# Kernel tuning notes

Measured on AMD Instinct MI355X. Metric: run time of the kernel, lower is better.

## Reference

```python
import jax, jax.numpy as jnp
import numpy as np

NUM_CLASSES = 1000
GAMMA = 0.9
N = 131072


def setup_inputs() -> dict:
    key = jax.random.key(0)
    k1, k2, k3 = jax.random.split(key, 3)
    preds = jax.random.normal(k1, (N, NUM_CLASSES), dtype=jnp.float32)
    labels = jax.random.randint(k2, (N,), 0, NUM_CLASSES)
    val_preds = jax.random.normal(k3, (NUM_CLASSES, NUM_CLASSES), dtype=jnp.float32)
    return {"preds": preds, "labels": labels, "val_preds": val_preds}


def reference(preds, labels, val_preds):
    # Equivalent of ValScores.update: per-class mean of preds (label-indexed
    # segment reduction) followed by an EMA update, skipping empty classes.
    C = val_preds.shape[0]
    # sums[c] = sum of preds rows with label c   -> [C, C]
    sums = jax.ops.segment_sum(preds, labels, num_segments=C)
    # counts[c] = number of rows with label c    -> [C]
    counts = jax.ops.segment_sum(jnp.ones((preds.shape[0],), preds.dtype),
                                 labels, num_segments=C)
    has = counts > 0
    means = sums / jnp.where(has, counts, jnp.ones_like(counts))[:, None]
    new_val = jnp.where(has[:, None],
                        (1.0 - GAMMA) * means + GAMMA * val_preds,
                        val_preds)
    return new_val
```

## Files before the change

kernel.cpp:

```cpp
#include <hip/hip_runtime.h>

#define NUM_C 1000
#define COLS4 250
#define GAMMA 0.9f

__global__ void count_kernel(const int* __restrict__ labels,
                             int* __restrict__ counts, int n) {
    int i = blockIdx.x * blockDim.x + threadIdx.x;
    int stride = gridDim.x * blockDim.x;
    for (; i < n; i += stride) {
        atomicAdd(&counts[labels[i]], 1);
    }
}

__global__ void scan_kernel(const int* __restrict__ counts,
                            int* __restrict__ offsets) {
    __shared__ int s[1024];
    int tid = threadIdx.x;
    int v = (tid < NUM_C) ? counts[tid] : 0;
    s[tid] = v;
    __syncthreads();
    for (int d = 1; d < 1024; d <<= 1) {
        int x = (tid >= d) ? s[tid - d] : 0;
        __syncthreads();
        s[tid] += x;
        __syncthreads();
    }
    if (tid < NUM_C) offsets[tid] = s[tid] - v;
}

__global__ void scatter_kernel(const int* __restrict__ labels,
                               const int* __restrict__ offsets,
                               int* __restrict__ cursors,
                               int* __restrict__ rowidx, int n) {
    int i = blockIdx.x * blockDim.x + threadIdx.x;
    int stride = gridDim.x * blockDim.x;
    for (; i < n; i += stride) {
        int l = labels[i];
        int pos = offsets[l] + atomicAdd(&cursors[l], 1);
        rowidx[pos] = i;
    }
}

__global__ __launch_bounds__(128) void accum_kernel(
        const float* __restrict__ preds, const float* __restrict__ val,
        const int* __restrict__ counts, const int* __restrict__ offsets,
        const int* __restrict__ rowidx, float* __restrict__ out) {
    const int c    = blockIdx.x;
    const int tid  = threadIdx.x;
    const int col4 = blockIdx.y * 125 + tid;
    const bool active = (tid < 125);

    const float4* __restrict__ pv = (const float4*)preds;
    const float4* __restrict__ vv = (const float4*)val;
    float4* __restrict__ ov = (float4*)out;
    const size_t crow = (size_t)c * COLS4;

    const int nc  = counts[c];
    const int off = offsets[c];

    if (nc == 0) {
        if (active) ov[crow + col4] = vv[crow + col4];
        return;
    }

    __shared__ int rows_s[1024];
    float4 acc = {0.f, 0.f, 0.f, 0.f};

    for (int base = 0; base < nc; base += 1024) {
        int m = min(nc - base, 1024);
        for (int j = tid; j < m; j += 128) rows_s[j] = rowidx[off + base + j];
        __syncthreads();

        int r = 0;
        for (; r + 4 <= m; r += 4) {
            size_t i0 = (size_t)rows_s[r + 0] * COLS4;
            size_t i1 = (size_t)rows_s[r + 1] * COLS4;
            size_t i2 = (size_t)rows_s[r + 2] * COLS4;
            size_t i3 = (size_t)rows_s[r + 3] * COLS4;
            if (active) {
                float4 v0 = pv[i0 + col4];
                float4 v1 = pv[i1 + col4];
                float4 v2 = pv[i2 + col4];
                float4 v3 = pv[i3 + col4];
                acc.x += (v0.x + v1.x) + (v2.x + v3.x);
                acc.y += (v0.y + v1.y) + (v2.y + v3.y);
                acc.z += (v0.z + v1.z) + (v2.z + v3.z);
                acc.w += (v0.w + v1.w) + (v2.w + v3.w);
            }
        }
        for (; r < m; r++) {
            size_t i0 = (size_t)rows_s[r] * COLS4;
            if (active) {
                float4 v0 = pv[i0 + col4];
                acc.x += v0.x; acc.y += v0.y; acc.z += v0.z; acc.w += v0.w;
            }
        }
        __syncthreads();
    }

    if (active) {
        float inv = 1.0f / (float)nc;
        float4 vp = vv[crow + col4];
        float4 o;
        o.x = (1.0f - GAMMA) * (acc.x * inv) + GAMMA * vp.x;
        o.y = (1.0f - GAMMA) * (acc.y * inv) + GAMMA * vp.y;
        o.z = (1.0f - GAMMA) * (acc.z * inv) + GAMMA * vp.z;
        o.w = (1.0f - GAMMA) * (acc.w * inv) + GAMMA * vp.w;
        ov[crow + col4] = o;
    }
}

extern "C" void kernel_launch(void* const* d_in, const int* in_sizes, int n_in,
                              void* d_out, int out_size, void* d_ws, size_t ws_size,
                              hipStream_t stream) {
    const float* preds  = (const float*)d_in[0];
    const int*   labels = (const int*)d_in[1];
    const float* val    = (const float*)d_in[2];
    float*       out    = (float*)d_out;
    const int n = in_sizes[1];

    char* ws = (char*)d_ws;
    int* counts  = (int*)(ws + 0);
    int* offsets = (int*)(ws + 4096);
    int* cursors = (int*)(ws + 8192);
    int* rowidx  = (int*)(ws + 12288);

    hipMemsetAsync(d_ws, 0, 12288, stream);
    count_kernel<<<256, 256, 0, stream>>>(labels, counts, n);
    scan_kernel<<<1, 1024, 0, stream>>>(counts, offsets);
    scatter_kernel<<<256, 256, 0, stream>>>(labels, offsets, cursors, rowidx, n);
    accum_kernel<<<dim3(NUM_C, 2), 128, 0, stream>>>(preds, val, counts, offsets,
                                                     rowidx, out);
}
```

Before: 731.9 us.

## Use one 256-thread block per class with 8-way nontemporal loads and dual accumulators

The accumulation kernel now uses one 256-thread block per class covering all 250 float4 columns, instead of two 128-thread blocks each covering half. The row loop is unrolled to 8 rows, with two accumulators and nontemporal loads, so more loads are in flight and the streamed preds rows bypass cache retention. The count and scatter kernels switch from grid-stride loops to one thread per element. The grid halves to 1000 blocks, which may lower occupancy, and inactive lanes now issue loads against column 0 rather than being masked. These lanes are redundant but safe.

```diff
diff --git a/kernel.cpp b/kernel.cpp
--- a/kernel.cpp
+++ b/kernel.cpp
@@ -4,13 +4,12 @@
 #define COLS4 250
 #define GAMMA 0.9f
 
+typedef float v4f __attribute__((ext_vector_type(4)));
+
 __global__ void count_kernel(const int* __restrict__ labels,
                              int* __restrict__ counts, int n) {
     int i = blockIdx.x * blockDim.x + threadIdx.x;
-    int stride = gridDim.x * blockDim.x;
-    for (; i < n; i += stride) {
-        atomicAdd(&counts[labels[i]], 1);
-    }
+    if (i < n) atomicAdd(&counts[labels[i]], 1);
 }
 
 __global__ void scan_kernel(const int* __restrict__ counts,
@@ -34,26 +33,25 @@
                                int* __restrict__ cursors,
                                int* __restrict__ rowidx, int n) {
     int i = blockIdx.x * blockDim.x + threadIdx.x;
-    int stride = gridDim.x * blockDim.x;
-    for (; i < n; i += stride) {
+    if (i < n) {
         int l = labels[i];
         int pos = offsets[l] + atomicAdd(&cursors[l], 1);
         rowidx[pos] = i;
     }
 }
 
-__global__ __launch_bounds__(128) void accum_kernel(
+__global__ __launch_bounds__(256) void accum_kernel(
         const float* __restrict__ preds, const float* __restrict__ val,
         const int* __restrict__ counts, const int* __restrict__ offsets,
         const int* __restrict__ rowidx, float* __restrict__ out) {
-    const int c    = blockIdx.x;
-    const int tid  = threadIdx.x;
-    const int col4 = blockIdx.y * 125 + tid;
-    const bool active = (tid < 125);
+    const int c   = blockIdx.x;
+    const int tid = threadIdx.x;
+    const bool active = (tid < COLS4);
+    const int col4 = active ? tid : 0;
 
-    const float4* __restrict__ pv = (const float4*)preds;
-    const float4* __restrict__ vv = (const float4*)val;
-    float4* __restrict__ ov = (float4*)out;
+    const v4f* __restrict__ pv = (const v4f*)preds;
+    const v4f* __restrict__ vv = (const v4f*)val;
+    v4f* __restrict__ ov = (v4f*)out;
     const size_t crow = (size_t)c * COLS4;
 
     const int nc  = counts[c];
@@ -64,49 +62,49 @@
         return;
     }
 
-    __shared__ int rows_s[1024];
-    float4 acc = {0.f, 0.f, 0.f, 0.f};
+    __shared__ int rows_s[512];
+    v4f acc0 = {0.f, 0.f, 0.f, 0.f};
+    v4f acc1 = {0.f, 0.f, 0.f, 0.f};
 
-    for (int base = 0; base < nc; base += 1024) {
-        int m = min(nc - base, 1024);
-        for (int j = tid; j < m; j += 128) rows_s[j] = rowidx[off + base + j];
+    for (int base = 0; base < nc; base += 512) {
+        int m = min(nc - base, 512);
+        if (tid < m) rows_s[tid] = rowidx[off + base + tid];
+        if (tid + 256 < m) rows_s[tid + 256] = rowidx[off + base + tid + 256];
         __syncthreads();
 
         int r = 0;
-        for (; r + 4 <= m; r += 4) {
-            size_t i0 = (size_t)rows_s[r + 0] * COLS4;
-            size_t i1 = (size_t)rows_s[r + 1] * COLS4;
-            size_t i2 = (size_t)rows_s[r + 2] * COLS4;
-            size_t i3 = (size_t)rows_s[r + 3] * COLS4;
-            if (active) {
-                float4 v0 = pv[i0 + col4];
-                float4 v1 = pv[i1 + col4];
-                float4 v2 = pv[i2 + col4];
-                float4 v3 = pv[i3 + col4];
-                acc.x += (v0.x + v1.x) + (v2.x + v3.x);
-                acc.y += (v0.y + v1.y) + (v2.y + v3.y);
-                acc.z += (v0.z + v1.z) + (v2.z + v3.z);
-                acc.w += (v0.w + v1.w) + (v2.w + v3.w);
-            }
+        for (; r + 8 <= m; r += 8) {
+            size_t i0 = (size_t)rows_s[r + 0] * COLS4 + col4;
+            size_t i1 = (size_t)rows_s[r + 1] * COLS4 + col4;
+            size_t i2 = (size_t)rows_s[r + 2] * COLS4 + col4;
+            size_t i3 = (size_t)rows_s[r + 3] * COLS4 + col4;
+            size_t i4 = (size_t)rows_s[r + 4] * COLS4 + col4;
+            size_t i5 = (size_t)rows_s[r + 5] * COLS4 + col4;
+            size_t i6 = (size_t)rows_s[r + 6] * COLS4 + col4;
+            size_t i7 = (size_t)rows_s[r + 7] * COLS4 + col4;
+            v4f v0 = __builtin_nontemporal_load(&pv[i0]);
+            v4f v1 = __builtin_nontemporal_load(&pv[i1]);
+            v4f v2 = __builtin_nontemporal_load(&pv[i2]);
+            v4f v3 = __builtin_nontemporal_load(&pv[i3]);
+            v4f v4 = __builtin_nontemporal_load(&pv[i4]);
+            v4f v5 = __builtin_nontemporal_load(&pv[i5]);
+            v4f v6 = __builtin_nontemporal_load(&pv[i6]);
+            v4f v7 = __builtin_nontemporal_load(&pv[i7]);
+            acc0 += (v0 + v1) + (v2 + v3);
+            acc1 += (v4 + v5) + (v6 + v7);
         }
         for (; r < m; r++) {
-            size_t i0 = (size_t)rows_s[r] * COLS4;
-            if (active) {
-                float4 v0 = pv[i0 + col4];
-                acc.x += v0.x; acc.y += v0.y; acc.z += v0.z; acc.w += v0.w;
-            }
+            size_t i0 = (size_t)rows_s[r] * COLS4 + col4;
+            acc0 += __builtin_nontemporal_load(&pv[i0]);
         }
         __syncthreads();
     }
 
     if (active) {
         float inv = 1.0f / (float)nc;
-        float4 vp = vv[crow + col4];
-        float4 o;
-        o.x = (1.0f - GAMMA) * (acc.x * inv) + GAMMA * vp.x;
-        o.y = (1.0f - GAMMA) * (acc.y * inv) + GAMMA * vp.y;
-        o.z = (1.0f - GAMMA) * (acc.z * inv) + GAMMA * vp.z;
-        o.w = (1.0f - GAMMA) * (acc.w * inv) + GAMMA * vp.w;
+        v4f s = acc0 + acc1;
+        v4f vp = vv[crow + col4];
+        v4f o = (1.0f - GAMMA) * (s * inv) + GAMMA * vp;
         ov[crow + col4] = o;
     }
 }
@@ -126,10 +124,9 @@
     int* cursors = (int*)(ws + 8192);
     int* rowidx  = (int*)(ws + 12288);
 
-    hipMemsetAsync(d_ws, 0, 12288, stream);
-    count_kernel<<<256, 256, 0, stream>>>(labels, counts, n);
+    (void)hipMemsetAsync(d_ws, 0, 12288, stream);
+    count_kernel<<<(n + 255) / 256, 256, 0, stream>>>(labels, counts, n);
     scan_kernel<<<1, 1024, 0, stream>>>(counts, offsets);
-    scatter_kernel<<<256, 256, 0, stream>>>(labels, offsets, cursors, rowidx, n);
-    accum_kernel<<<dim3(NUM_C, 2), 128, 0, stream>>>(preds, val, counts, offsets,
-                                                     rowidx, out);
+    scatter_kernel<<<(n + 255) / 256, 256, 0, stream>>>(labels, offsets, cursors, rowidx, n);
+    accum_kernel<<<NUM_C, 256, 0, stream>>>(preds, val, counts, offsets, rowidx, out);
 }
```

Result: faster. 706.6 us (-3.5%).
